# Kernel tuning notes

Measured on AMD Instinct MI355X. Metric: run time of the kernel, lower is better.

Reference implementation:

```python
import jax, jax.numpy as jnp
import numpy as np
from jax import lax

DIM = 128
DEPTH = 2
OUT_DIM = 256
DIM_HEAD = 64
HEADS = 8
WS = 16
INNER = DIM_HEAD * HEADS
EPS = 1e-5
SCALE = DIM_HEAD ** (-0.5)


def setup_inputs() -> dict:
    key = jax.random.key(0)
    ks = jax.random.split(key, 20)
    s = 0.02
    L = DEPTH
    inp = {
        "x": jax.random.normal(ks[0], (1, DIM, 256, 256), dtype=jnp.float32),
        "ln1_g": jnp.ones((L, DIM), dtype=jnp.float32),
        "ln1_b": jnp.zeros((L, DIM), dtype=jnp.float32),
        "wq": jax.random.normal(ks[1], (L, INNER, DIM), dtype=jnp.float32) * s,
        "wkv": jax.random.normal(ks[2], (L, 2 * INNER, DIM), dtype=jnp.float32) * s,
        "wo": jax.random.normal(ks[3], (L, DIM, INNER), dtype=jnp.float32) * s,
        "bo": jnp.zeros((L, DIM), dtype=jnp.float32),
        "ln2_g": jnp.ones((L, DIM), dtype=jnp.float32),
        "ln2_b": jnp.zeros((L, DIM), dtype=jnp.float32),
        "w_in": jax.random.normal(ks[4], (L, DIM, DIM), dtype=jnp.float32) * s,
        "b_in": jnp.zeros((L, DIM), dtype=jnp.float32),
        "w_c3": jax.random.normal(ks[5], (L, OUT_DIM, DIM, 3, 3), dtype=jnp.float32) * s,
        "b_c3": jnp.zeros((L, OUT_DIM), dtype=jnp.float32),
        "w_c1": jax.random.normal(ks[6], (L, DIM, OUT_DIM), dtype=jnp.float32) * s,
        "b_c1": jnp.zeros((L, DIM), dtype=jnp.float32),
        "w_outer": jax.random.normal(ks[7], (DIM, DIM), dtype=jnp.float32) * s,
        "b_outer": jnp.zeros((DIM,), dtype=jnp.float32),
    }
    return inp


def _layernorm(x, g, b):
    # channel-wise (dim=1) norm; note torch code uses (std + eps), not sqrt(var + eps)
    mean = jnp.mean(x, axis=1, keepdims=True)
    std = jnp.sqrt(jnp.var(x, axis=1, keepdims=True))
    return (x - mean) / (std + EPS) * g[None, :, None, None] + b[None, :, None, None]


def _conv1x1(w, x, b=None):
    y = jnp.einsum('oi,bihw->bohw', w, x)
    if b is not None:
        y = y + b[None, :, None, None]
    return y


def _to_windows(t, B, H, W):
    # [B, HEADS*DIM_HEAD, H, W] -> [B*HEADS*nx*ny, WS*WS, DIM_HEAD]
    nx, ny = H // WS, W // WS
    t = t.reshape(B, HEADS, DIM_HEAD, nx, WS, ny, WS)
    t = t.transpose(0, 1, 3, 5, 4, 6, 2)
    return t.reshape(B * HEADS * nx * ny, WS * WS, DIM_HEAD)


def _from_windows(t, B, H, W):
    nx, ny = H // WS, W // WS
    t = t.reshape(B, HEADS, nx, ny, WS, WS, DIM_HEAD)
    t = t.transpose(0, 1, 6, 2, 4, 3, 5)
    return t.reshape(B, HEADS * DIM_HEAD, H, W)


def _attention(x, wq_l, wkv_l, wo_l, bo_l):
    B, _, H, W = x.shape
    q = _conv1x1(wq_l, x)
    kv = _conv1x1(wkv_l, x)
    k, v = kv[:, :INNER], kv[:, INNER:]
    q = _to_windows(q, B, H, W)
    k = _to_windows(k, B, H, W)
    v = _to_windows(v, B, H, W)
    sim = jnp.einsum('bid,bjd->bij', q, k) * SCALE  # [nwin, 256, 256]
    attn = jax.nn.softmax(sim, axis=-1)
    out = jnp.einsum('bij,bjd->bid', attn, v)
    out = _from_windows(out, B, H, W)
    return _conv1x1(wo_l, out, bo_l)


def _feedforward(x, w_in_l, b_in_l, w_c3_l, b_c3_l, w_c1_l, b_c1_l):
    h = _conv1x1(w_in_l, x, b_in_l)
    h = lax.conv_general_dilated(h, w_c3_l, window_strides=(1, 1), padding='SAME',
                                 dimension_numbers=('NCHW', 'OIHW', 'NCHW'))
    h = h + b_c3_l[None, :, None, None]
    h = jax.nn.gelu(h, approximate=False)
    return _conv1x1(w_c1_l, h, b_c1_l)


def reference(x, ln1_g, ln1_b, wq, wkv, wo, bo, ln2_g, ln2_b,
              w_in, b_in, w_c3, b_c3, w_c1, b_c1, w_outer, b_outer):
    for l in range(DEPTH):
        xn = _layernorm(x, ln1_g[l], ln1_b[l])
        x = _attention(xn, wq[l], wkv[l], wo[l], bo[l]) + x
        xn = _layernorm(x, ln2_g[l], ln2_b[l])
        x = _feedforward(xn, w_in[l], b_in[l], w_c3[l], b_c3[l], w_c1[l], b_c1[l]) + x
    return _conv1x1(w_outer, x, b_outer) + x
```

## Files before the change

### kernel.cpp

```cpp
#include <hip/hip_runtime.h>
#include <hip/hip_bf16.h>
#include <math.h>

typedef __hip_bfloat16 bf16;
typedef float f4 __attribute__((ext_vector_type(4)));
typedef short s8 __attribute__((ext_vector_type(8)));
typedef unsigned int u2 __attribute__((ext_vector_type(2)));
typedef unsigned int u4v __attribute__((ext_vector_type(4)));

__device__ __forceinline__ void gload16(const void* g, char* l) {
  __builtin_amdgcn_global_load_lds(
      (const __attribute__((address_space(1))) unsigned int*)g,
      (__attribute__((address_space(3))) unsigned int*)l, 16, 0, 0);
}
__device__ __forceinline__ unsigned short bfr(float f) {
  bf16 h = __float2bfloat16(f);
  return *(unsigned short*)&h;
}
__device__ __forceinline__ unsigned int pk2(float a, float b) {
  return (unsigned int)bfr(a) | ((unsigned int)bfr(b) << 16);
}
__device__ __forceinline__ unsigned int pkt(float a, float b) {
  return __builtin_amdgcn_perm(__float_as_uint(b), __float_as_uint(a), 0x07060302u);
}

__global__ __launch_bounds__(256) void prep_w(
    const float* __restrict__ wq, const float* __restrict__ wkv,
    const float* __restrict__ wo, const float* __restrict__ win,
    const float* __restrict__ wc3, const float* __restrict__ wc1,
    const float* __restrict__ wout, ushort* __restrict__ cw)
{
  int i = blockIdx.x * 256 + threadIdx.x;
  float v;
  if (i < 131072) v = wq[i];
  else if (i < 393216) v = wkv[i - 131072];
  else if (i < 524288) v = wo[i - 393216];
  else if (i < 1146880) return;
  else if (i < 1212416) v = wc1[i - 1146880];
  else if (i < 1228800) v = wout[i - 1212416];
  else if (i < 1230848) { cw[i] = 0; return; }
  else return;
  cw[i] = bfr(v);
}

__global__ __launch_bounds__(128) void prep_fold(
    const float* __restrict__ wc3, const float* __restrict__ win,
    const float* __restrict__ b_in, ushort* __restrict__ cw3out,
    float* __restrict__ T)
{
  __shared__ float col[128][9];
  __shared__ float sred[2][9];
  const int lyr = blockIdx.x >> 8, m = blockIdx.x & 255;
  const int tid = threadIdx.x;
  const float* src = wc3 + (((size_t)lyr * 256 + m) * 128 + tid) * 9;
#pragma unroll
  for (int t = 0; t < 9; ++t) col[tid][t] = src[t];
  float bi = b_in[lyr * 128 + tid];
  float sb[9];
#pragma unroll
  for (int t = 0; t < 9; ++t) {
    float v = col[tid][t] * bi;
    v += __shfl_xor(v, 1, 64);  v += __shfl_xor(v, 2, 64);
    v += __shfl_xor(v, 4, 64);  v += __shfl_xor(v, 8, 64);
    v += __shfl_xor(v, 16, 64); v += __shfl_xor(v, 32, 64);
    sb[t] = v;
  }
  if ((tid & 63) == 0) {
#pragma unroll
    for (int t = 0; t < 9; ++t) sred[tid >> 6][t] = sb[t];
  }
  __syncthreads();
  float acc[9] = {0.f,0.f,0.f,0.f,0.f,0.f,0.f,0.f,0.f};
  const float* wrow = win + (size_t)lyr * 16384 + tid;
  for (int c = 0; c < 128; ++c) {
    float wv = wrow[(size_t)c * 128];
#pragma unroll
    for (int t = 0; t < 9; ++t) acc[t] += col[c][t] * wv;
  }
  ushort* dst = cw3out + (size_t)lyr * 294912 + (size_t)m * 1152 + tid;
#pragma unroll
  for (int t = 0; t < 9; ++t) dst[t * 128] = bfr(acc[t]);
  if (tid == 0) {
    float s[9];
#pragma unroll
    for (int t = 0; t < 9; ++t) s[t] = sred[0][t] + sred[1][t];
    float* Tl = T + lyr * 2304;
    Tl[0 * 256 + m] = s[0]+s[1]+s[2]+s[3]+s[4]+s[5]+s[6]+s[7]+s[8];
    Tl[1 * 256 + m] = s[0] + s[1] + s[2];
    Tl[2 * 256 + m] = s[6] + s[7] + s[8];
    Tl[3 * 256 + m] = s[0] + s[3] + s[6];
    Tl[4 * 256 + m] = s[2] + s[5] + s[8];
    Tl[5 * 256 + m] = s[0];
    Tl[6 * 256 + m] = s[2];
    Tl[7 * 256 + m] = s[6];
    Tl[8 * 256 + m] = s[8];
  }
}

template<bool NCHW>
__global__ __launch_bounds__(256) void ln_nhwc(
    const float* __restrict__ x, const float* __restrict__ g,
    const float* __restrict__ b, ushort* __restrict__ y)
{
  const int p = blockIdx.x * 256 + threadIdx.x;
  f4 v[32];
  float s = 0.f, s2 = 0.f;
  if constexpr (NCHW) {
#pragma unroll
    for (int i = 0; i < 32; ++i)
#pragma unroll
      for (int j = 0; j < 4; ++j) {
        float t = x[(size_t)(i * 4 + j) * 65536 + p];
        v[i][j] = t; s += t; s2 += t * t;
      }
  } else {
    const f4* base = (const f4*)(x + (size_t)p * 128);
#pragma unroll
    for (int i = 0; i < 32; ++i) {
      v[i] = base[i];
#pragma unroll
      for (int j = 0; j < 4; ++j) { s += v[i][j]; s2 += v[i][j] * v[i][j]; }
    }
  }
  float mean = s * (1.f / 128.f);
  float var = s2 * (1.f / 128.f) - mean * mean;
  var = var > 0.f ? var : 0.f;
  float inv = 1.f / (sqrtf(var) + 1e-5f);
  u2* dst = (u2*)(y + (size_t)p * 128);
#pragma unroll
  for (int i = 0; i < 32; ++i) {
    f4 gg = *(const f4*)(g + i * 4);
    f4 bb = *(const f4*)(b + i * 4);
    float f0 = (v[i][0] - mean) * inv * gg[0] + bb[0];
    float f1 = (v[i][1] - mean) * inv * gg[1] + bb[1];
    float f2 = (v[i][2] - mean) * inv * gg[2] + bb[2];
    float f3 = (v[i][3] - mean) * inv * gg[3] + bb[3];
    u2 st; st.x = pk2(f0, f1); st.y = pk2(f2, f3);
    dst[i] = st;
  }
}

template<int MODE>
__global__ __launch_bounds__(256) void gemm_nhwc(
    const ushort* __restrict__ A, const ushort* __restrict__ X,
    const float* __restrict__ bias, const float* __restrict__ res,
    void* __restrict__ out, ushort* __restrict__ out2,
    const float* __restrict__ lng, const float* __restrict__ lnb,
    ushort* __restrict__ xn, const int K, const int M)
{
  __shared__ __align__(16) char sm[32768];
  const int tid = threadIdx.x, w = tid >> 6, l = tid & 63;
  const int quad = l >> 4, l15 = l & 15;
  const int n0 = blockIdx.x * 128, m0 = blockIdx.y * 128;
  const int mh = (w & 1) * 64, nh = (w >> 1) * 64;
  const f4 fz = {0.f, 0.f, 0.f, 0.f};
  f4 acc[4][4];
#pragma unroll
  for (int a = 0; a < 4; ++a)
#pragma unroll
    for (int b2 = 0; b2 < 4; ++b2) acc[a][b2] = fz;

  const int KI = K >> 6;
  for (int kk = 0; kk < KI; ++kk) {
    if (kk) __syncthreads();
    const int k0 = kk << 6;
#pragma unroll
    for (int j = 0; j < 4; ++j) {
      int p = j * 256 + tid, r = p >> 3, c = (p & 7) ^ (r & 7);
      gload16(A + (size_t)(m0 + r) * K + k0 + c * 8, sm + (j * 256 + w * 64) * 16);
    }
#pragma unroll
    for (int j = 0; j < 4; ++j) {
      int p = j * 256 + tid, r = p >> 3, c = (p & 7) ^ (r & 7);
      gload16(X + (size_t)(n0 + r) * K + k0 + c * 8, sm + 16384 + (j * 256 + w * 64) * 16);
    }
    __syncthreads();
#pragma unroll
    for (int ks = 0; ks < 2; ++ks) {
      s8 af[4], bx[4];
#pragma unroll
      for (int mt = 0; mt < 4; ++mt) {
        int rr = mh + mt * 16 + l15;
        af[mt] = *(const s8*)(sm + rr * 128 + (((ks * 4 + quad) ^ (rr & 7)) << 4));
      }
#pragma unroll
      for (int nt = 0; nt < 4; ++nt) {
        int rr = nh + nt * 16 + l15;
        bx[nt] = *(const s8*)(sm + 16384 + rr * 128 + (((ks * 4 + quad) ^ (rr & 7)) << 4));
      }
#pragma unroll
      for (int mt = 0; mt < 4; ++mt)
#pragma unroll
        for (int nt = 0; nt < 4; ++nt)
          acc[mt][nt] = __builtin_amdgcn_mfma_f32_16x16x32_bf16(af[mt], bx[nt], acc[mt][nt], 0, 0, 0);
    }
  }

  if constexpr (MODE == 5 || MODE == 6) {
    float s1[4] = {0.f, 0.f, 0.f, 0.f}, s2[4] = {0.f, 0.f, 0.f, 0.f};
#pragma unroll
    for (int mt = 0; mt < 4; ++mt) {
      const int m = mh + mt * 16 + quad * 4;
      f4 bb = *(const f4*)(bias + m);
#pragma unroll
      for (int nt = 0; nt < 4; ++nt) {
        const int n = n0 + nh + nt * 16 + l15;
        f4 v = acc[mt][nt] + bb;
        if constexpr (MODE == 5) {
          f4 r = *(const f4*)(res + (size_t)n * 128 + m);
          v += r;
        } else {
          f4 r;
#pragma unroll
          for (int i = 0; i < 4; ++i) r[i] = res[(size_t)(m + i) * 65536 + n];
          v += r;
        }
        *(f4*)((float*)out + (size_t)n * 128 + m) = v;
        acc[mt][nt] = v;
        s1[nt] += v[0] + v[1] + v[2] + v[3];
        s2[nt] += v[0] * v[0] + v[1] * v[1] + v[2] * v[2] + v[3] * v[3];
      }
    }
    __syncthreads();
    float* pb = (float*)sm;
#pragma unroll
    for (int nt = 0; nt < 4; ++nt) {
      float a1 = s1[nt], a2 = s2[nt];
      a1 += __shfl_xor(a1, 16, 64); a1 += __shfl_xor(a1, 32, 64);
      a2 += __shfl_xor(a2, 16, 64); a2 += __shfl_xor(a2, 32, 64);
      s1[nt] = a1; s2[nt] = a2;
      if (quad == 0) {
        int pn = nh + nt * 16 + l15;
        pb[((w & 1) * 128 + pn) * 2]     = a1;
        pb[((w & 1) * 128 + pn) * 2 + 1] = a2;
      }
    }
    __syncthreads();
#pragma unroll
    for (int nt = 0; nt < 4; ++nt) {
      int pn = nh + nt * 16 + l15;
      float t1 = s1[nt] + pb[((1 - (w & 1)) * 128 + pn) * 2];
      float t2 = s2[nt] + pb[((1 - (w & 1)) * 128 + pn) * 2 + 1];
      float mean = t1 * (1.f / 128.f);
      float var = t2 * (1.f / 128.f) - mean * mean;
      var = var > 0.f ? var : 0.f;
      s1[nt] = mean;
      s2[nt] = 1.f / (sqrtf(var) + 1e-5f);
    }
#pragma unroll
    for (int mt = 0; mt < 4; ++mt) {
      const int m = mh + mt * 16 + quad * 4;
      f4 gg = *(const f4*)(lng + m);
      f4 b2 = *(const f4*)(lnb + m);
#pragma unroll
      for (int nt = 0; nt < 4; ++nt) {
        const int n = n0 + nh + nt * 16 + l15;
        f4 v = acc[mt][nt];
        float mean = s1[nt], inv = s2[nt];
        float f0 = (v[0] - mean) * inv * gg[0] + b2[0];
        float f1 = (v[1] - mean) * inv * gg[1] + b2[1];
        float f2 = (v[2] - mean) * inv * gg[2] + b2[2];
        float f3 = (v[3] - mean) * inv * gg[3] + b2[3];
        u2 st; st.x = pk2(f0, f1); st.y = pk2(f2, f3);
        *(u2*)(xn + (size_t)n * 128 + m) = st;
      }
    }
    return;
  }

#pragma unroll
  for (int mt = 0; mt < 4; ++mt) {
#pragma unroll
    for (int nt = 0; nt < 4; ++nt) {
      const int m = m0 + mh + mt * 16 + quad * 4;
      const int n = n0 + nh + nt * 16 + l15;
      f4 bb = *(const f4*)(bias + m);
      f4 v = acc[mt][nt] + bb;
      if constexpr (MODE == 0) {
        u2 st; st.x = pk2(v[0], v[1]); st.y = pk2(v[2], v[3]);
        *(u2*)((ushort*)out + (size_t)n * M + m) = st;
      } else if constexpr (MODE == 1 || MODE == 3) {
        f4 r = *(const f4*)(res + (size_t)n * M + m);
        v += r;
        *(f4*)((float*)out + (size_t)n * M + m) = v;
        if constexpr (MODE == 3) {
          u2 st; st.x = pk2(v[0], v[1]); st.y = pk2(v[2], v[3]);
          *(u2*)(out2 + (size_t)n * M + m) = st;
        }
      } else if constexpr (MODE == 4) {
        f4 r;
#pragma unroll
        for (int i = 0; i < 4; ++i) r[i] = res[(size_t)(m + i) * 65536 + n];
        v += r;
        *(f4*)((float*)out + (size_t)n * M + m) = v;
      } else {
        f4 r = *(const f4*)(res + (size_t)n * M + m);
#pragma unroll
        for (int i = 0; i < 4; ++i)
          ((float*)out)[(size_t)(m + i) * 65536 + n] = v[i] + r[i];
      }
    }
  }
}

__global__ __launch_bounds__(256) void conv3_kernel(
    const ushort* __restrict__ A, const ushort* __restrict__ X,
    const float* __restrict__ bias, ushort* __restrict__ out,
    const ushort* __restrict__ zp, const float* __restrict__ T)
{
  __shared__ __align__(16) char sm[32768];
  const int tid = threadIdx.x, w = tid >> 6, l = tid & 63;
  const int quad = l >> 4, l15 = l & 15;
  const int n0 = blockIdx.x * 128, m0 = blockIdx.y * 128;
  const int mh = (w & 1) * 64, nh = (w >> 1) * 64;
  const f4 fz = {0.f, 0.f, 0.f, 0.f};
  f4 acc[4][4];
#pragma unroll
  for (int a = 0; a < 4; ++a)
#pragma unroll
    for (int b2 = 0; b2 < 4; ++b2) acc[a][b2] = fz;

  for (int kk = 0; kk < 18; ++kk) {
    if (kk) __syncthreads();
    const int tap = kk >> 1, ky = tap / 3, kx = tap - ky * 3;
    const int dn = (ky - 1) * 256 + (kx - 1);
    const int kseg = (kk & 1) << 6;
#pragma unroll
    for (int j = 0; j < 4; ++j) {
      int p = j * 256 + tid, r = p >> 3, c = (p & 7) ^ (r & 7);
      gload16(A + (size_t)(m0 + r) * 1152 + kk * 64 + c * 8, sm + (j * 256 + w * 64) * 16);
    }
#pragma unroll
    for (int j = 0; j < 4; ++j) {
      int p = j * 256 + tid, r = p >> 3, c = (p & 7) ^ (r & 7);
      int nl = n0 + r;
      int ys = (nl >> 8) + ky - 1, xs = (nl & 255) + kx - 1;
      const ushort* gp = ((unsigned)ys < 256u && (unsigned)xs < 256u)
                         ? X + (size_t)(nl + dn) * 128 + kseg + c * 8 : zp;
      gload16(gp, sm + 16384 + (j * 256 + w * 64) * 16);
    }
    __syncthreads();
#pragma unroll
    for (int ks = 0; ks < 2; ++ks) {
      s8 af[4], bx[4];
#pragma unroll
      for (int mt = 0; mt < 4; ++mt) {
        int rr = mh + mt * 16 + l15;
        af[mt] = *(const s8*)(sm + rr * 128 + (((ks * 4 + quad) ^ (rr & 7)) << 4));
      }
#pragma unroll
      for (int nt = 0; nt < 4; ++nt) {
        int rr = nh + nt * 16 + l15;
        bx[nt] = *(const s8*)(sm + 16384 + rr * 128 + (((ks * 4 + quad) ^ (rr & 7)) << 4));
      }
#pragma unroll
      for (int mt = 0; mt < 4; ++mt)
#pragma unroll
        for (int nt = 0; nt < 4; ++nt)
          acc[mt][nt] = __builtin_amdgcn_mfma_f32_16x16x32_bf16(af[mt], bx[nt], acc[mt][nt], 0, 0, 0);
    }
  }
  const int y = n0 >> 8;
  const bool y0 = (y == 0), y1 = (y == 255);
  const int xbase = (n0 & 255) + nh;
#pragma unroll
  for (int mt = 0; mt < 4; ++mt) {
    const int m = m0 + mh + mt * 16 + quad * 4;
    f4 base = *(const f4*)(bias + m) + *(const f4*)(T + m);
    f4 Lc = *(const f4*)(T + 3 * 256 + m);
    f4 Rc = *(const f4*)(T + 4 * 256 + m);
    if (y0) {
      base -= *(const f4*)(T + 1 * 256 + m);
      Lc -= *(const f4*)(T + 5 * 256 + m);
      Rc -= *(const f4*)(T + 6 * 256 + m);
    }
    if (y1) {
      base -= *(const f4*)(T + 2 * 256 + m);
      Lc -= *(const f4*)(T + 7 * 256 + m);
      Rc -= *(const f4*)(T + 8 * 256 + m);
    }
#pragma unroll
    for (int nt = 0; nt < 4; ++nt) {
      const int n = n0 + nh + nt * 16 + l15;
      const int x = xbase + nt * 16 + l15;
      float fx0 = (x == 0) ? 1.f : 0.f;
      float fx1 = (x == 255) ? 1.f : 0.f;
      f4 v = acc[mt][nt] + base - Lc * fx0 - Rc * fx1;
      float g0 = 0.5f * v[0] * (1.f + erff(v[0] * 0.70710678118f));
      float g1 = 0.5f * v[1] * (1.f + erff(v[1] * 0.70710678118f));
      float g2 = 0.5f * v[2] * (1.f + erff(v[2] * 0.70710678118f));
      float g3 = 0.5f * v[3] * (1.f + erff(v[3] * 0.70710678118f));
      u2 st; st.x = pk2(g0, g1); st.y = pk2(g2, g3);
      *(u2*)(out + (size_t)n * 256 + m) = st;
    }
  }
}

__global__ __launch_bounds__(512) void attn_kernel(
    const ushort* __restrict__ xn, const ushort* __restrict__ wq,
    const ushort* __restrict__ wkv, ushort* __restrict__ ao)
{
  __shared__ __align__(16) char sm[147456];
  const int tid = threadIdx.x, w = tid >> 6, l = tid & 63;
  const int quad = l >> 4, l15 = l & 15;
  const int win = blockIdx.x, head = blockIdx.y;
  const int nbase = ((win >> 4) << 12) + ((win & 15) << 4);
  char* RX  = sm;
  char* RW  = sm + 65536;
  char* RK  = sm + 114688;
  char* RVT = sm;
  char* Pw  = sm + 32768 + w * 4096;
  char* RO  = RW;
  const f4 fz = {0.f, 0.f, 0.f, 0.f};

#pragma unroll
  for (int j = 0; j < 8; ++j) {
    int p = j * 512 + tid, r = p >> 4, c = (p & 15) ^ (r & 15);
    int n = nbase + ((r >> 4) << 8) + (r & 15);
    gload16(xn + (size_t)n * 128 + c * 8, RX + (j * 512 + w * 64) * 16);
  }
  {
    const ushort* wpq = wq + (size_t)head * 64 * 128;
    const ushort* wpk = wkv + (size_t)head * 64 * 128;
    const ushort* wpv = wkv + (size_t)(512 + head * 64) * 128;
#pragma unroll
    for (int j = 0; j < 2; ++j) {
      int p = j * 512 + tid, r = p >> 4, c = (p & 15) ^ (r & 15);
      gload16(wpq + (size_t)r * 128 + c * 8, RW + (j * 512 + w * 64) * 16);
    }
#pragma unroll
    for (int j = 0; j < 2; ++j) {
      int p = j * 512 + tid, r = p >> 4, c = (p & 15) ^ (r & 15);
      gload16(wpk + (size_t)r * 128 + c * 8, RW + 16384 + (j * 512 + w * 64) * 16);
    }
#pragma unroll
    for (int j = 0; j < 2; ++j) {
      int p = j * 512 + tid, r = p >> 4, c = (p & 15) ^ (r & 15);
      gload16(wpv + (size_t)r * 128 + c * 8, RW + 32768 + (j * 512 + w * 64) * 16);
    }
  }
  __syncthreads();

  s8 bq[2][2];
  {
    f4 acc[4][2];
#pragma unroll
    for (int a = 0; a < 4; ++a) { acc[a][0] = fz; acc[a][1] = fz; }
#pragma unroll
    for (int ks = 0; ks < 4; ++ks) {
      s8 af[4], bx[2];
#pragma unroll
      for (int mt = 0; mt < 4; ++mt) {
        int rr = mt * 16 + l15;
        af[mt] = *(const s8*)(RW + rr * 256 + (((ks * 4 + quad) ^ (rr & 15)) << 4));
      }
#pragma unroll
      for (int nt = 0; nt < 2; ++nt) {
        int rr = w * 32 + nt * 16 + l15;
        bx[nt] = *(const s8*)(RX + rr * 256 + (((ks * 4 + quad) ^ (rr & 15)) << 4));
      }
#pragma unroll
      for (int mt = 0; mt < 4; ++mt)
#pragma unroll
        for (int nt = 0; nt < 2; ++nt)
          acc[mt][nt] = __builtin_amdgcn_mfma_f32_16x16x32_bf16(af[mt], bx[nt], acc[mt][nt], 0, 0, 0);
    }
#pragma unroll
    for (int nt = 0; nt < 2; ++nt) {
      unsigned pd[4][2];
#pragma unroll
      for (int mt = 0; mt < 4; ++mt) {
        pd[mt][0] = pkt(acc[mt][nt][0], acc[mt][nt][1]);
        pd[mt][1] = pkt(acc[mt][nt][2], acc[mt][nt][3]);
      }
#pragma unroll
      for (int ks = 0; ks < 2; ++ks) {
        u4v t;
#pragma unroll
        for (int dj = 0; dj < 4; ++dj) {
          int srcl = l15 + (((quad & 1) * 2 + (dj >> 1)) << 4);
          unsigned va = (unsigned)__shfl((int)pd[2 * ks][dj & 1], srcl, 64);
          unsigned vb = (unsigned)__shfl((int)pd[2 * ks + 1][dj & 1], srcl, 64);
          t[dj] = (quad < 2) ? va : vb;
        }
        bq[nt][ks] = __builtin_bit_cast(s8, t);
      }
    }
  }

  {
    f4 acc[4][2];
#pragma unroll
    for (int a = 0; a < 4; ++a) { acc[a][0] = fz; acc[a][1] = fz; }
#pragma unroll
    for (int ks = 0; ks < 4; ++ks) {
      s8 af[4], bx[2];
#pragma unroll
      for (int mt = 0; mt < 4; ++mt) {
        int rr = mt * 16 + l15;
        af[mt] = *(const s8*)(RW + 16384 + rr * 256 + (((ks * 4 + quad) ^ (rr & 15)) << 4));
      }
#pragma unroll
      for (int nt = 0; nt < 2; ++nt) {
        int rr = w * 32 + nt * 16 + l15;
        bx[nt] = *(const s8*)(RX + rr * 256 + (((ks * 4 + quad) ^ (rr & 15)) << 4));
      }
#pragma unroll
      for (int mt = 0; mt < 4; ++mt)
#pragma unroll
        for (int nt = 0; nt < 2; ++nt)
          acc[mt][nt] = __builtin_amdgcn_mfma_f32_16x16x32_bf16(af[mt], bx[nt], acc[mt][nt], 0, 0, 0);
    }
#pragma unroll
    for (int mt = 0; mt < 4; ++mt)
#pragma unroll
      for (int nt = 0; nt < 2; ++nt) {
        int tok = w * 32 + nt * 16 + l15, d0 = mt * 16 + quad * 4;
        char* a = RK + tok * 128 + (((d0 >> 3) ^ (tok & 7)) << 4) + (d0 & 7) * 2;
        *(unsigned int*)a = pkt(acc[mt][nt][0], acc[mt][nt][1]);
        *(unsigned int*)(a + 4) = pkt(acc[mt][nt][2], acc[mt][nt][3]);
      }
  }

  {
    f4 acc[2][4];
#pragma unroll
    for (int a = 0; a < 2; ++a)
#pragma unroll
      for (int b2 = 0; b2 < 4; ++b2) acc[a][b2] = fz;
#pragma unroll
    for (int ks = 0; ks < 4; ++ks) {
      s8 ax[2], bw[4];
#pragma unroll
      for (int mt = 0; mt < 2; ++mt) {
        int rr = w * 32 + mt * 16 + l15;
        ax[mt] = *(const s8*)(RX + rr * 256 + (((ks * 4 + quad) ^ (rr & 15)) << 4));
      }
#pragma unroll
      for (int nt = 0; nt < 4; ++nt) {
        int rr = nt * 16 + l15;
        bw[nt] = *(const s8*)(RW + 32768 + rr * 256 + (((ks * 4 + quad) ^ (rr & 15)) << 4));
      }
#pragma unroll
      for (int mt = 0; mt < 2; ++mt)
#pragma unroll
        for (int nt = 0; nt < 4; ++nt)
          acc[mt][nt] = __builtin_amdgcn_mfma_f32_16x16x32_bf16(ax[mt], bw[nt], acc[mt][nt], 0, 0, 0);
    }
    __syncthreads();
#pragma unroll
    for (int mt = 0; mt < 2; ++mt)
#pragma unroll
      for (int nt = 0; nt < 4; ++nt) {
        int d = nt * 16 + l15, t0 = w * 32 + mt * 16 + quad * 4;
        char* a = RVT + d * 512 + (((t0 >> 3) ^ (d & 31)) << 4) + (t0 & 7) * 2;
        *(unsigned int*)a = pkt(acc[mt][nt][0], acc[mt][nt][1]);
        *(unsigned int*)(a + 4) = pkt(acc[mt][nt][2], acc[mt][nt][3]);
      }
  }
  __syncthreads();

  f4 o[4][2];
  float lsum[2] = {0.f, 0.f};
#pragma unroll
  for (int a = 0; a < 4; ++a) { o[a][0] = fz; o[a][1] = fz; }

  for (int jt = 0; jt < 4; ++jt) {
    f4 s[4][2];
#pragma unroll
    for (int a = 0; a < 4; ++a) { s[a][0] = fz; s[a][1] = fz; }
#pragma unroll
    for (int ks = 0; ks < 2; ++ks) {
      s8 af[4];
#pragma unroll
      for (int mt = 0; mt < 4; ++mt) {
        int rr = jt * 64 + mt * 16 + l15;
        af[mt] = *(const s8*)(RK + rr * 128 + (((ks * 4 + quad) ^ (rr & 7)) << 4));
      }
      __builtin_amdgcn_s_setprio(1);
#pragma unroll
      for (int mt = 0; mt < 4; ++mt)
#pragma unroll
        for (int nt = 0; nt < 2; ++nt)
          s[mt][nt] = __builtin_amdgcn_mfma_f32_16x16x32_bf16(af[mt], bq[nt][ks], s[mt][nt], 0, 0, 0);
      __builtin_amdgcn_s_setprio(0);
    }
#pragma unroll
    for (int mt = 0; mt < 4; ++mt)
#pragma unroll
      for (int nt = 0; nt < 2; ++nt) {
        float p0 = exp2f(s[mt][nt][0] * 0.18033688f);
        float p1 = exp2f(s[mt][nt][1] * 0.18033688f);
        float p2 = exp2f(s[mt][nt][2] * 0.18033688f);
        float p3 = exp2f(s[mt][nt][3] * 0.18033688f);
        lsum[nt] += p0 + p1 + p2 + p3;
        int iL = nt * 16 + l15, j0 = mt * 16 + quad * 4;
        char* a = Pw + iL * 128 + (((j0 >> 3) ^ (iL & 7)) << 4) + (j0 & 7) * 2;
        *(unsigned int*)a = pkt(p0, p1);
        *(unsigned int*)(a + 4) = pkt(p2, p3);
      }
#pragma unroll
    for (int ks = 0; ks < 2; ++ks) {
      s8 av[4], bp[2];
#pragma unroll
      for (int mt = 0; mt < 4; ++mt) {
        int d = mt * 16 + l15;
        av[mt] = *(const s8*)(RVT + d * 512 + (((jt * 8 + ks * 4 + quad) ^ (d & 31)) << 4));
      }
#pragma unroll
      for (int nt = 0; nt < 2; ++nt) {
        int iL = nt * 16 + l15;
        bp[nt] = *(const s8*)(Pw + iL * 128 + (((ks * 4 + quad) ^ (iL & 7)) << 4));
      }
      __builtin_amdgcn_s_setprio(1);
#pragma unroll
      for (int mt = 0; mt < 4; ++mt)
#pragma unroll
        for (int nt = 0; nt < 2; ++nt)
          o[mt][nt] = __builtin_amdgcn_mfma_f32_16x16x32_bf16(av[mt], bp[nt], o[mt][nt], 0, 0, 0);
      __builtin_amdgcn_s_setprio(0);
    }
  }

  float inv[2];
#pragma unroll
  for (int nt = 0; nt < 2; ++nt) {
    float v = lsum[nt];
    v += __shfl_xor(v, 16, 64);
    v += __shfl_xor(v, 32, 64);
    inv[nt] = 1.f / v;
  }
#pragma unroll
  for (int mt = 0; mt < 4; ++mt)
#pragma unroll
    for (int nt = 0; nt < 2; ++nt) {
      int i = w * 32 + nt * 16 + l15, d0 = mt * 16 + quad * 4;
      char* a = RO + i * 128 + (((d0 >> 3) ^ (i & 7)) << 4) + (d0 & 7) * 2;
      *(unsigned int*)a = pkt(o[mt][nt][0] * inv[nt], o[mt][nt][1] * inv[nt]);
      *(unsigned int*)(a + 4) = pkt(o[mt][nt][2] * inv[nt], o[mt][nt][3] * inv[nt]);
    }
  __syncthreads();
  const int tok = tid >> 1, half = tid & 1;
  const int n = nbase + ((tok >> 4) << 8) + (tok & 15);
  ushort* dst = ao + (size_t)n * 512 + head * 64 + half * 32;
#pragma unroll
  for (int c = 0; c < 4; ++c) {
    u4v v = *(const u4v*)(RO + tok * 128 + (((half * 4 + c) ^ (tok & 7)) << 4));
    *(u4v*)(dst + c * 8) = v;
  }
}

extern "C" void kernel_launch(void* const* d_in, const int* in_sizes, int n_in,
                              void* d_out, int out_size, void* d_ws, size_t ws_size,
                              hipStream_t stream)
{
  const float* x_in    = (const float*)d_in[0];
  const float* ln1_g   = (const float*)d_in[1];
  const float* ln1_b   = (const float*)d_in[2];
  const float* wq      = (const float*)d_in[3];
  const float* wkv     = (const float*)d_in[4];
  const float* wo      = (const float*)d_in[5];
  const float* bo      = (const float*)d_in[6];
  const float* ln2_g   = (const float*)d_in[7];
  const float* ln2_b   = (const float*)d_in[8];
  const float* w_in    = (const float*)d_in[9];
  const float* b_in    = (const float*)d_in[10];
  const float* w_c3    = (const float*)d_in[11];
  const float* b_c3    = (const float*)d_in[12];
  const float* w_c1    = (const float*)d_in[13];
  const float* b_c1    = (const float*)d_in[14];
  const float* w_outer = (const float*)d_in[15];
  const float* b_outer = (const float*)d_in[16];

  char* wsb = (char*)d_ws;
  ushort* CW = (ushort*)wsb;
  float*  TB = (float*)(wsb + 3145728);
  float*  XH = (float*)(wsb + 4194304);
  ushort* XN = (ushort*)(wsb + 37748736);
  ushort* AO = (ushort*)(wsb + 54525952);
  ushort* G  = (ushort*)(wsb + 138412032);
  ushort* XB = (ushort*)(wsb + 171966464);

  const ushort* zp = CW + 1228800;
  dim3 b256(256);

  prep_w<<<dim3(4808), b256, 0, stream>>>(wq, wkv, wo, w_in, w_c3, w_c1, w_outer, CW);
  prep_fold<<<dim3(512), dim3(128), 0, stream>>>(w_c3, w_in, b_in, CW + 557056, TB);

  ln_nhwc<true><<<dim3(256), b256, 0, stream>>>(x_in, ln1_g, ln1_b, XN);
  attn_kernel<<<dim3(256, 8), dim3(512), 0, stream>>>(XN, CW, CW + 131072, AO);
  gemm_nhwc<6><<<dim3(512, 1), b256, 0, stream>>>(CW + 393216, AO, bo, x_in, XH,
      nullptr, ln2_g, ln2_b, XN, 512, 128);
  conv3_kernel<<<dim3(512, 2), b256, 0, stream>>>(CW + 557056, XN, b_c3, G, zp, TB);
  gemm_nhwc<5><<<dim3(512, 1), b256, 0, stream>>>(CW + 1146880, G, b_c1, XH, XH,
      nullptr, ln1_g + 128, ln1_b + 128, XN, 256, 128);

  attn_kernel<<<dim3(256, 8), dim3(512), 0, stream>>>(XN, CW + 65536, CW + 262144, AO);
  gemm_nhwc<5><<<dim3(512, 1), b256, 0, stream>>>(CW + 458752, AO, bo + 128, XH, XH,
      nullptr, ln2_g + 128, ln2_b + 128, XN, 512, 128);
  conv3_kernel<<<dim3(512, 2), b256, 0, stream>>>(CW + 851968, XN, b_c3 + 256, G, zp, TB + 2304);
  gemm_nhwc<3><<<dim3(512, 1), b256, 0, stream>>>(CW + 1179648, G, b_c1 + 128, XH, XH,
      XB, nullptr, nullptr, nullptr, 256, 128);

  gemm_nhwc<2><<<dim3(512, 1), b256, 0, stream>>>(CW + 1212416, XB, b_outer, XH, d_out,
      nullptr, nullptr, nullptr, nullptr, 128, 128);
}
```

Before: 620.9 us.

## Fuse final FFN conv1x1 and outer conv1x1 into one GEMM kernel

Adds a MODE 7 GEMM path that computes the last FFN 1x1 projection plus residual, stages the bf16 result in shared memory, and immediately multiplies it by the outer 1x1 weights before writing the NCHW output. This removes one kernel launch plus the global round trip of the intermediate bf16 tensor and an extra read of the fp32 residual. In exchange it doubles shared memory for that kernel to 64KB, which may reduce occupancy, and it keeps a second accumulator set live, raising register pressure.

After: 576.4 us, median of 2. 7.2% less time.

```diff
diff --git a/kernel.cpp b/kernel.cpp
--- a/kernel.cpp
+++ b/kernel.cpp
@@ -145,10 +145,12 @@
     const ushort* __restrict__ A, const ushort* __restrict__ X,
     const float* __restrict__ bias, const float* __restrict__ res,
     void* __restrict__ out, ushort* __restrict__ out2,
+    const ushort* __restrict__ A2,
     const float* __restrict__ lng, const float* __restrict__ lnb,
     ushort* __restrict__ xn, const int K, const int M)
 {
-  __shared__ __align__(16) char sm[32768];
+  constexpr unsigned SMSZ = (MODE == 7) ? 65536u : 32768u;
+  __shared__ __align__(16) char sm[SMSZ];
   const int tid = threadIdx.x, w = tid >> 6, l = tid & 63;
   const int quad = l >> 4, l15 = l & 15;
   const int n0 = blockIdx.x * 128, m0 = blockIdx.y * 128;
@@ -194,6 +196,74 @@
         for (int nt = 0; nt < 4; ++nt)
           acc[mt][nt] = __builtin_amdgcn_mfma_f32_16x16x32_bf16(af[mt], bx[nt], acc[mt][nt], 0, 0, 0);
     }
+  }
+
+  if constexpr (MODE == 7) {
+#pragma unroll
+    for (int mt = 0; mt < 4; ++mt) {
+      const int m = mh + mt * 16 + quad * 4;
+      f4 bb = *(const f4*)(bias + m);
+      const int seg = m >> 6, kl = m & 63;
+#pragma unroll
+      for (int nt = 0; nt < 4; ++nt) {
+        const int r = nh + nt * 16 + l15;
+        f4 v = acc[mt][nt] + bb + *(const f4*)(res + (size_t)(n0 + r) * 128 + m);
+        acc[mt][nt] = v;
+        u2 st; st.x = pk2(v[0], v[1]); st.y = pk2(v[2], v[3]);
+        *(u2*)(sm + 32768 + seg * 16384 + r * 128 +
+               (((kl >> 3) ^ (r & 7)) << 4) + (kl & 7) * 2) = st;
+      }
+    }
+    __syncthreads();
+#pragma unroll
+    for (int kk2 = 0; kk2 < 2; ++kk2)
+#pragma unroll
+      for (int j = 0; j < 4; ++j) {
+        int p = j * 256 + tid, r = p >> 3, c = (p & 7) ^ (r & 7);
+        gload16(A2 + (size_t)r * 128 + kk2 * 64 + c * 8,
+                sm + kk2 * 16384 + (j * 256 + w * 64) * 16);
+      }
+    __syncthreads();
+    f4 acc2[4][4];
+#pragma unroll
+    for (int a = 0; a < 4; ++a)
+#pragma unroll
+      for (int b2 = 0; b2 < 4; ++b2) acc2[a][b2] = fz;
+#pragma unroll
+    for (int kk2 = 0; kk2 < 2; ++kk2)
+#pragma unroll
+      for (int ks = 0; ks < 2; ++ks) {
+        s8 af[4], bx[4];
+#pragma unroll
+        for (int mt = 0; mt < 4; ++mt) {
+          int rr = mh + mt * 16 + l15;
+          af[mt] = *(const s8*)(sm + kk2 * 16384 + rr * 128 + (((ks * 4 + quad) ^ (rr & 7)) << 4));
+        }
+#pragma unroll
+        for (int nt = 0; nt < 4; ++nt) {
+          int rr = nh + nt * 16 + l15;
+          bx[nt] = *(const s8*)(sm + 32768 + kk2 * 16384 + rr * 128 + (((ks * 4 + quad) ^ (rr & 7)) << 4));
+        }
+#pragma unroll
+        for (int mt = 0; mt < 4; ++mt)
+#pragma unroll
+          for (int nt = 0; nt < 4; ++nt)
+            acc2[mt][nt] = __builtin_amdgcn_mfma_f32_16x16x32_bf16(af[mt], bx[nt], acc2[mt][nt], 0, 0, 0);
+      }
+#pragma unroll
+    for (int mt = 0; mt < 4; ++mt) {
+      const int m = mh + mt * 16 + quad * 4;
+      f4 bo2 = *(const f4*)(lng + m);
+#pragma unroll
+      for (int nt = 0; nt < 4; ++nt) {
+        const int n = n0 + nh + nt * 16 + l15;
+        f4 v2 = acc2[mt][nt] + bo2 + acc[mt][nt];
+#pragma unroll
+        for (int i = 0; i < 4; ++i)
+          ((float*)out)[(size_t)(m + i) * 65536 + n] = v2[i];
+      }
+    }
+    return;
   }
 
   if constexpr (MODE == 5 || MODE == 6) {
@@ -679,7 +749,6 @@
   ushort* XN = (ushort*)(wsb + 37748736);
   ushort* AO = (ushort*)(wsb + 54525952);
   ushort* G  = (ushort*)(wsb + 138412032);
-  ushort* XB = (ushort*)(wsb + 171966464);
 
   const ushort* zp = CW + 1228800;
   dim3 b256(256);
@@ -690,18 +759,15 @@
   ln_nhwc<true><<<dim3(256), b256, 0, stream>>>(x_in, ln1_g, ln1_b, XN);
   attn_kernel<<<dim3(256, 8), dim3(512), 0, stream>>>(XN, CW, CW + 131072, AO);
   gemm_nhwc<6><<<dim3(512, 1), b256, 0, stream>>>(CW + 393216, AO, bo, x_in, XH,
-      nullptr, ln2_g, ln2_b, XN, 512, 128);
+      nullptr, nullptr, ln2_g, ln2_b, XN, 512, 128);
   conv3_kernel<<<dim3(512, 2), b256, 0, stream>>>(CW + 557056, XN, b_c3, G, zp, TB);
   gemm_nhwc<5><<<dim3(512, 1), b256, 0, stream>>>(CW + 1146880, G, b_c1, XH, XH,
-      nullptr, ln1_g + 128, ln1_b + 128, XN, 256, 128);
+      nullptr, nullptr, ln1_g + 128, ln1_b + 128, XN, 256, 128);
 
   attn_kernel<<<dim3(256, 8), dim3(512), 0, stream>>>(XN, CW + 65536, CW + 262144, AO);
   gemm_nhwc<5><<<dim3(512, 1), b256, 0, stream>>>(CW + 458752, AO, bo + 128, XH, XH,
-      nullptr, ln2_g + 128, ln2_b + 128, XN, 512, 128);
+      nullptr, nullptr, ln2_g + 128, ln2_b + 128, XN, 512, 128);
   conv3_kernel<<<dim3(512, 2), b256, 0, stream>>>(CW + 851968, XN, b_c3 + 256, G, zp, TB + 2304);
-  gemm_nhwc<3><<<dim3(512, 1), b256, 0, stream>>>(CW + 1179648, G, b_c1 + 128, XH, XH,
-      XB, nullptr, nullptr, nullptr, 256, 128);
-
-  gemm_nhwc<2><<<dim3(512, 1), b256, 0, stream>>>(CW + 1212416, XB, b_outer, XH, d_out,
-      nullptr, nullptr, nullptr, nullptr, 128, 128);
-}
+  gemm_nhwc<7><<<dim3(512, 1), b256, 0, stream>>>(CW + 1179648, G, b_c1 + 128, XH, d_out,
+      nullptr, CW + 1212416, b_outer, nullptr, nullptr, 256, 128);
+}
```
